# Kernel tuning notes

Hardware: AMD Instinct MI355X
Metric: run time of the kernel (lower is better)

Reference implementation:

```python
import jax, jax.numpy as jnp
import numpy as np

NUM_GROUPS = 32


def setup_inputs() -> dict:
    key = jax.random.key(0)
    x = jax.random.normal(key, (16384, 4096), dtype=jnp.float32)
    return {"x": x}


def reference(x):
    N, D = x.shape
    G = NUM_GROUPS
    d = D // G
    # [N, G, d] -> mean-center over batch
    xg = x.reshape(N, G, d)
    xg = xg - xg.mean(axis=0, keepdims=True)
    # [G, N, d]
    xg = jnp.transpose(xg, (1, 0, 2))
    # per-group covariance: [G, d, d]
    covs = jnp.einsum('gnd,gne->gde', xg, xg) / (N - 1)
    S, U = jnp.linalg.eigh(covs)  # S: [G, d], U: [G, d, d]
    # whitening transform W = U diag(S^-1/2) U^T : [G, d, d]
    W = jnp.einsum('gde,ge,gfe->gdf', U, jax.lax.rsqrt(S), U)
    out = jnp.einsum('gnd,gdf->gnf', xg, W)  # [G, N, d]
    return jnp.transpose(out, (1, 0, 2)).reshape(N, D)
```

## Files before the change

kernel.cpp:

```cpp
#include <hip/hip_runtime.h>
#include <cstddef>

#define NROWS 16384
#define NCOLS 4096
#define NG 32
#define GD 128
#define NPC 16

typedef float f32x4 __attribute__((ext_vector_type(4)));
typedef short bf16x8 __attribute__((ext_vector_type(8)));

__device__ inline unsigned short f2bf(float f) {
    unsigned int u = __builtin_bit_cast(unsigned int, f);
    u += 0x7fffu + ((u >> 16) & 1u);
    return (unsigned short)(u >> 16);
}

__global__ __launch_bounds__(512) void k_cov(
    const float* __restrict__ x, float* __restrict__ xtx, float* __restrict__ ps,
    unsigned short* __restrict__ xhi)
{
    __shared__ unsigned short xt[2][128][42];
    __shared__ float red[8][128];
    const int bid = blockIdx.x;
    const int g = bid >> 4, p = bid & 15;
    const int t = threadIdx.x;
    const int w = t >> 6;
    const int lane = t & 63;
    const int f2 = lane;
    const int lm = lane & 15, lk = lane >> 4;
    const float* xb = x + (size_t)(p * 1024) * NCOLS + g * GD + 2 * f2;
    unsigned int* xo = (unsigned int*)(xhi
        + ((size_t)g * NROWS + p * 1024 + w * 4) * GD + 2 * f2);

    float csum0 = 0.f, csum1 = 0.f;
    f32x4 acc[8];
#pragma unroll
    for (int ni = 0; ni < 8; ++ni) acc[ni] = (f32x4){0.f, 0.f, 0.f, 0.f};

    float2 v[4];
#define CLOAD(CC) \
    _Pragma("unroll") for (int i = 0; i < 4; ++i) \
        v[i] = *(const float2*)(xb + (size_t)((CC) * 32 + w * 4 + i) * NCOLS);
#define CWRITE(BUF, CC) { \
    ushort4 h0, h1; \
    unsigned short* hp0 = (unsigned short*)&h0; \
    unsigned short* hp1 = (unsigned short*)&h1; \
    _Pragma("unroll") for (int i = 0; i < 4; ++i) { \
        csum0 += v[i].x; csum1 += v[i].y; \
        unsigned int b0 = f2bf(v[i].x), b1 = f2bf(v[i].y); \
        hp0[i] = (unsigned short)b0; hp1[i] = (unsigned short)b1; \
        xo[(size_t)((CC) * 32 + i) * 64] = b0 | (b1 << 16); } \
    *(ushort4*)&xt[BUF][2 * f2][w * 4] = h0; \
    *(ushort4*)&xt[BUF][2 * f2 + 1][w * 4] = h1; }

    CLOAD(0);
    CWRITE(0, 0);
    __syncthreads();

    for (int c = 0; c < 32; ++c) {
        const int cur = c & 1;
        if (c < 31) { CLOAD(c + 1); }
        bf16x8 A0 = *(const bf16x8*)&xt[cur][w * 16 + lm][lk * 8];
        bf16x8 B[8];
#pragma unroll
        for (int n = 0; n < 8; ++n)
            B[n] = *(const bf16x8*)&xt[cur][n * 16 + lm][lk * 8];
#pragma unroll
        for (int n = 0; n < 8; ++n)
            acc[n] = __builtin_amdgcn_mfma_f32_16x16x32_bf16(A0, B[n], acc[n], 0, 0, 0);
        if (c < 31) { CWRITE(cur ^ 1, c + 1); }
        __syncthreads();
    }
#undef CLOAD
#undef CWRITE

    float* ob = xtx + (size_t)bid * (GD * GD);
#pragma unroll
    for (int ni = 0; ni < 8; ++ni) {
        const int i0 = w * 16 + lk * 4;
        const int j = ni * 16 + lm;
#pragma unroll
        for (int r = 0; r < 4; ++r)
            ob[(size_t)(i0 + r) * GD + j] = acc[ni][r];
    }
    red[w][2 * f2] = csum0;
    red[w][2 * f2 + 1] = csum1;
    __syncthreads();
    if (t < 128) {
        float s = 0.f;
#pragma unroll
        for (int r = 0; r < 8; ++r) s += red[r][t];
        ps[(size_t)bid * GD + t] = s;
    }
}

__global__ __launch_bounds__(256) void k_covreduce(
    const float* __restrict__ xtx, const float* __restrict__ ps,
    float* __restrict__ C)
{
    __shared__ float mu[128];
    const int bid = blockIdx.x;
    const int g = bid >> 4, s = bid & 15;
    const int t = threadIdx.x;
    if (t < 128) {
        float m = 0.f;
#pragma unroll
        for (int p = 0; p < NPC; ++p) m += ps[(size_t)(g * NPC + p) * GD + t];
        mu[t] = m * (1.0f / (float)NROWS);
    }
    __syncthreads();
    const int e = s * 1024 + t * 4;
    const int i = e >> 7, j = e & 127;
    float4 sum = make_float4(0.f, 0.f, 0.f, 0.f);
#pragma unroll
    for (int p = 0; p < NPC; ++p) {
        const float4 vv = *(const float4*)(xtx + ((size_t)(g * NPC + p) << 14) + e);
        sum.x += vv.x; sum.y += vv.y; sum.z += vv.z; sum.w += vv.w;
    }
    const float inv = 1.0f / (float)(NROWS - 1);
    const float mi2 = (float)NROWS * mu[i];
    float4 r;
    r.x = (sum.x - mi2 * mu[j + 0]) * inv;
    r.y = (sum.y - mi2 * mu[j + 1]) * inv;
    r.z = (sum.z - mi2 * mu[j + 2]) * inv;
    r.w = (sum.w - mi2 * mu[j + 3]) * inv;
    *(float4*)(C + (size_t)g * (GD * GD) + e) = r;
}

__global__ __launch_bounds__(256) void k_prep(
    const float* __restrict__ Cg, float* __restrict__ scale,
    float* __restrict__ Y0, float* __restrict__ Z0)
{
    __shared__ float Cs[128][129];
    __shared__ float rs[128];
    __shared__ float sinv[1];
    const int g = blockIdx.x;
    const int t = threadIdx.x;
    for (int k = 0; k < 64; ++k) {
        int e = t + 256 * k;
        Cs[e >> 7][e & 127] = Cg[(size_t)g * (GD * GD) + e];
    }
    __syncthreads();
    if (t < 128) {
        float s = 0.f;
        for (int i = 0; i < 128; ++i) s += fabsf(Cs[i][t]);
        rs[t] = s;
    }
    __syncthreads();
    if (t == 0) {
        float up = 0.f, lo = 1e30f;
        for (int i = 0; i < 128; ++i) {
            up = fmaxf(up, rs[i]);
            lo = fminf(lo, 2.0f * Cs[i][i] - rs[i]);
        }
        float c = 0.5f * (up + fmaxf(lo, 0.0f));
        c = fmaxf(c, 1e-20f);
        sinv[0] = 1.0f / c;
        scale[g] = rsqrtf(c);
    }
    __syncthreads();
    const float invc = sinv[0];
    for (int k = 0; k < 64; ++k) {
        int e = t + 256 * k;
        int i = e >> 7, j = e & 127;
        Y0[(size_t)g * (GD * GD) + e] = Cs[i][j] * invc;
        Z0[(size_t)g * (GD * GD) + e] = (i == j) ? 1.0f : 0.0f;
    }
}

__global__ __launch_bounds__(256) void k_ns_iter(
    const float* __restrict__ Yin, const float* __restrict__ Zin,
    float* __restrict__ Yout, float* __restrict__ Zout)
{
    __shared__ float Ys[128][132];
    __shared__ float Zs[128][132];
    __shared__ float Ts[128][16];
    const int bid = blockIdx.x;
    const int g = bid >> 3;
    const int sl = bid & 7;
    const int J0 = sl * 16;
    const int t = threadIdx.x;
    const float* Yg = Yin + (size_t)g * GD * GD;
    const float* Zg = Zin + (size_t)g * GD * GD;
#pragma unroll
    for (int k = 0; k < 16; ++k) {
        int q = t + 256 * k;
        int row = q >> 5, c4 = q & 31;
        *(float4*)&Ys[row][c4 * 4] = *(const float4*)(Yg + (size_t)q * 4);
        *(float4*)&Zs[row][c4 * 4] = *(const float4*)(Zg + (size_t)q * 4);
    }
    __syncthreads();
    const int i = t >> 1;
    const int jb = (t & 1) * 8;

    float accT[8];
#pragma unroll
    for (int q = 0; q < 8; ++q) accT[q] = 0.f;
    for (int k4 = 0; k4 < 32; ++k4) {
        float4 zv = *(const float4*)&Zs[i][k4 * 4];
        float zz[4] = {zv.x, zv.y, zv.z, zv.w};
#pragma unroll
        for (int e = 0; e < 4; ++e) {
            const int k = k4 * 4 + e;
            float4 y0 = *(const float4*)&Ys[k][J0 + jb];
            float4 y1 = *(const float4*)&Ys[k][J0 + jb + 4];
            float yy[8] = {y0.x, y0.y, y0.z, y0.w, y1.x, y1.y, y1.z, y1.w};
#pragma unroll
            for (int q = 0; q < 8; ++q) accT[q] = fmaf(zz[e], yy[q], accT[q]);
        }
    }
#pragma unroll
    for (int q = 0; q < 8; ++q) Ts[i][jb + q] = accT[q];
    __syncthreads();

    float ay[8], az[8];
#pragma unroll
    for (int q = 0; q < 8; ++q) { ay[q] = 0.f; az[q] = 0.f; }
    for (int k4 = 0; k4 < 32; ++k4) {
        float4 yv = *(const float4*)&Ys[i][k4 * 4];
        float4 zv = *(const float4*)&Zs[i][k4 * 4];
        float yy[4] = {yv.x, yv.y, yv.z, yv.w};
        float zz[4] = {zv.x, zv.y, zv.z, zv.w};
#pragma unroll
        for (int e = 0; e < 4; ++e) {
            const int k = k4 * 4 + e;
            float4 t0 = *(const float4*)&Ts[k][jb];
            float4 t1 = *(const float4*)&Ts[k][jb + 4];
            float tt[8] = {t0.x, t0.y, t0.z, t0.w, t1.x, t1.y, t1.z, t1.w};
#pragma unroll
            for (int q = 0; q < 8; ++q) {
                ay[q] = fmaf(yy[e], tt[q], ay[q]);
                az[q] = fmaf(zz[e], tt[q], az[q]);
            }
        }
    }
    float4 yc0 = *(const float4*)&Ys[i][J0 + jb];
    float4 yc1 = *(const float4*)&Ys[i][J0 + jb + 4];
    float4 zc0 = *(const float4*)&Zs[i][J0 + jb];
    float4 zc1 = *(const float4*)&Zs[i][J0 + jb + 4];
    float* Yo = Yout + (size_t)g * GD * GD + (size_t)i * GD + J0 + jb;
    float* Zo = Zout + (size_t)g * GD * GD + (size_t)i * GD + J0 + jb;
    *(float4*)(Yo)     = make_float4(1.5f*yc0.x - 0.5f*ay[0], 1.5f*yc0.y - 0.5f*ay[1],
                                     1.5f*yc0.z - 0.5f*ay[2], 1.5f*yc0.w - 0.5f*ay[3]);
    *(float4*)(Yo + 4) = make_float4(1.5f*yc1.x - 0.5f*ay[4], 1.5f*yc1.y - 0.5f*ay[5],
                                     1.5f*yc1.z - 0.5f*ay[6], 1.5f*yc1.w - 0.5f*ay[7]);
    *(float4*)(Zo)     = make_float4(1.5f*zc0.x - 0.5f*az[0], 1.5f*zc0.y - 0.5f*az[1],
                                     1.5f*zc0.z - 0.5f*az[2], 1.5f*zc0.w - 0.5f*az[3]);
    *(float4*)(Zo + 4) = make_float4(1.5f*zc1.x - 0.5f*az[4], 1.5f*zc1.y - 0.5f*az[5],
                                     1.5f*zc1.z - 0.5f*az[6], 1.5f*zc1.w - 0.5f*az[7]);
}

__global__ __launch_bounds__(256) void k_wprep(
    const float* __restrict__ Z, const float* __restrict__ scale,
    const float* __restrict__ ps,
    unsigned short* __restrict__ WT, float* __restrict__ muW)
{
    __shared__ float Zs[128][129];
    __shared__ float mu[128];
    const int g = blockIdx.x;
    const int t = threadIdx.x;
    const float sc = scale[g];
    if (t < 128) {
        float m = 0.f;
#pragma unroll
        for (int p = 0; p < NPC; ++p) m += ps[(size_t)(g * NPC + p) * GD + t];
        mu[t] = m * (1.0f / (float)NROWS);
    }
    for (int k = 0; k < 64; ++k) {
        int e = t + 256 * k;
        Zs[e >> 7][e & 127] = Z[(size_t)g * (GD * GD) + e];
    }
    __syncthreads();
    const int n = t & 127, kh = t >> 7;
    unsigned short* o = WT + (size_t)g * (GD * GD) + (size_t)n * GD + kh * 64;
    for (int k = 0; k < 64; k += 2) {
        unsigned int pk = (unsigned int)f2bf(Zs[kh * 64 + k][n] * sc)
                        | ((unsigned int)f2bf(Zs[kh * 64 + k + 1][n] * sc) << 16);
        *(unsigned int*)(o + k) = pk;
    }
    if (t < 128) {
        float s = 0.f;
        for (int d = 0; d < 128; ++d) s = fmaf(mu[d], Zs[d][t], s);
        muW[g * GD + t] = s * sc;
    }
}

__global__ __launch_bounds__(512) void k_apply(
    const unsigned short* __restrict__ xhi, const unsigned short* __restrict__ WT,
    const float* __restrict__ muW, float* __restrict__ out)
{
    __shared__ float tile[64][132];
    const int bid = blockIdx.x;
    const int g = bid & 31;
    const int rb = bid >> 5;
    const int t = threadIdx.x;
    const int lane = t & 63, w = t >> 6;
    const int lm = lane & 15, lk = lane >> 4;
    const int fq = w >> 1;
    const int sh = (w & 1) * 32;

    bf16x8 Wf[2][4];
    {
        const unsigned short* wg = WT + (size_t)g * (GD * GD);
#pragma unroll
        for (int fi = 0; fi < 2; ++fi)
#pragma unroll
            for (int ks = 0; ks < 4; ++ks)
                Wf[fi][ks] = *(const bf16x8*)(wg
                    + (size_t)(fq * 32 + fi * 16 + lm) * GD + ks * 32 + lk * 8);
    }
    float mw[2];
#pragma unroll
    for (int fi = 0; fi < 2; ++fi)
        mw[fi] = muW[g * GD + fq * 32 + fi * 16 + lm];

    const int row0 = rb * 64;
    const unsigned short* ab = xhi
        + ((size_t)g * NROWS + row0 + sh + lm) * GD + lk * 8;

    bf16x8 u[8];
#pragma unroll
    for (int ks = 0; ks < 4; ++ks) {
        u[ks * 2 + 0] = *(const bf16x8*)(ab + ks * 32);
        u[ks * 2 + 1] = *(const bf16x8*)(ab + (size_t)16 * GD + ks * 32);
    }

    f32x4 acc[2][2];
#pragma unroll
    for (int mi = 0; mi < 2; ++mi)
#pragma unroll
        for (int fi = 0; fi < 2; ++fi) acc[mi][fi] = (f32x4){0.f, 0.f, 0.f, 0.f};

#pragma unroll
    for (int ks = 0; ks < 4; ++ks) {
#pragma unroll
        for (int fi = 0; fi < 2; ++fi) {
            acc[0][fi] = __builtin_amdgcn_mfma_f32_16x16x32_bf16(
                u[ks * 2 + 0], Wf[fi][ks], acc[0][fi], 0, 0, 0);
            acc[1][fi] = __builtin_amdgcn_mfma_f32_16x16x32_bf16(
                u[ks * 2 + 1], Wf[fi][ks], acc[1][fi], 0, 0, 0);
        }
    }

#pragma unroll
    for (int mi = 0; mi < 2; ++mi)
#pragma unroll
        for (int fi = 0; fi < 2; ++fi)
#pragma unroll
            for (int r = 0; r < 4; ++r)
                tile[sh + mi * 16 + lk * 4 + r][fq * 32 + fi * 16 + lm]
                    = acc[mi][fi][r] - mw[fi];
    __syncthreads();

    const int srow = t >> 5;
    const int scol = (t & 31) * 4;
    float* obase = out + (size_t)row0 * NCOLS + g * GD;
#pragma unroll
    for (int p = 0; p < 4; ++p) {
        const int row = p * 16 + srow;
        float4 v = *(const float4*)&tile[row][scol];
        *(float4*)(obase + (size_t)row * NCOLS + scol) = v;
    }
}

extern "C" void kernel_launch(void* const* d_in, const int* in_sizes, int n_in,
                              void* d_out, int out_size, void* d_ws, size_t ws_size,
                              hipStream_t stream) {
    const float* x = (const float*)d_in[0];
    float* out = (float*)d_out;
    float* ws = (float*)d_ws;

    float* xtx   = ws;
    float* ps    = xtx + (size_t)NG * NPC * GD * GD;
    float* scale = ps + (size_t)NG * NPC * GD;
    float* Cbuf  = scale + 32;
    float* Ya    = Cbuf + (size_t)NG * GD * GD;
    float* Za    = Ya + (size_t)NG * GD * GD;
    float* Yb    = Za + (size_t)NG * GD * GD;
    float* Zb    = Yb + (size_t)NG * GD * GD;
    float* muW   = Zb + (size_t)NG * GD * GD;
    unsigned short* WT  = (unsigned short*)(muW + NCOLS);
    unsigned short* xhi = WT + (size_t)NG * GD * GD;

    k_cov<<<NG * NPC, 512, 0, stream>>>(x, xtx, ps, xhi);
    k_covreduce<<<NG * NPC, 256, 0, stream>>>(xtx, ps, Cbuf);
    k_prep<<<NG, 256, 0, stream>>>(Cbuf, scale, Ya, Za);
    for (int it = 0; it < 5; ++it) {
        if ((it & 1) == 0)
            k_ns_iter<<<NG * 8, 256, 0, stream>>>(Ya, Za, Yb, Zb);
        else
            k_ns_iter<<<NG * 8, 256, 0, stream>>>(Yb, Zb, Ya, Za);
    }
    k_wprep<<<NG, 256, 0, stream>>>(Zb, scale, ps, WT, muW);
    k_apply<<<NG * 256, 512, 0, stream>>>(xhi, WT, muW, out);
}
```

Measured before the change: 340.1 us.

## Drop bf16 staging copy of x; apply reads fp32 x directly, fewer NS iterations

The covariance kernel no longer writes a bf16 transposed copy of x. The apply kernel instead reads the fp32 input directly and converts it to bf16 in registers before the MFMA, with smaller 256-thread blocks covering 32 rows each. This removes a 128MB write and the matching read, at the cost of reading 256MB of fp32 in apply. Separately, the Newton-Schulz iteration count drops from 5 to 4, which cuts work but may reduce the accuracy of the inverse square root.

```diff
diff --git a/kernel.cpp b/kernel.cpp
--- a/kernel.cpp
+++ b/kernel.cpp
@@ -17,8 +17,7 @@
 }
 
 __global__ __launch_bounds__(512) void k_cov(
-    const float* __restrict__ x, float* __restrict__ xtx, float* __restrict__ ps,
-    unsigned short* __restrict__ xhi)
+    const float* __restrict__ x, float* __restrict__ xtx, float* __restrict__ ps)
 {
     __shared__ unsigned short xt[2][128][42];
     __shared__ float red[8][128];
@@ -30,8 +29,6 @@
     const int f2 = lane;
     const int lm = lane & 15, lk = lane >> 4;
     const float* xb = x + (size_t)(p * 1024) * NCOLS + g * GD + 2 * f2;
-    unsigned int* xo = (unsigned int*)(xhi
-        + ((size_t)g * NROWS + p * 1024 + w * 4) * GD + 2 * f2);
 
     float csum0 = 0.f, csum1 = 0.f;
     f32x4 acc[8];
@@ -42,20 +39,18 @@
 #define CLOAD(CC) \
     _Pragma("unroll") for (int i = 0; i < 4; ++i) \
         v[i] = *(const float2*)(xb + (size_t)((CC) * 32 + w * 4 + i) * NCOLS);
-#define CWRITE(BUF, CC) { \
+#define CWRITE(BUF) { \
     ushort4 h0, h1; \
     unsigned short* hp0 = (unsigned short*)&h0; \
     unsigned short* hp1 = (unsigned short*)&h1; \
     _Pragma("unroll") for (int i = 0; i < 4; ++i) { \
         csum0 += v[i].x; csum1 += v[i].y; \
-        unsigned int b0 = f2bf(v[i].x), b1 = f2bf(v[i].y); \
-        hp0[i] = (unsigned short)b0; hp1[i] = (unsigned short)b1; \
-        xo[(size_t)((CC) * 32 + i) * 64] = b0 | (b1 << 16); } \
+        hp0[i] = f2bf(v[i].x); hp1[i] = f2bf(v[i].y); } \
     *(ushort4*)&xt[BUF][2 * f2][w * 4] = h0; \
     *(ushort4*)&xt[BUF][2 * f2 + 1][w * 4] = h1; }
 
     CLOAD(0);
-    CWRITE(0, 0);
+    CWRITE(0);
     __syncthreads();
 
     for (int c = 0; c < 32; ++c) {
@@ -69,7 +64,7 @@
 #pragma unroll
         for (int n = 0; n < 8; ++n)
             acc[n] = __builtin_amdgcn_mfma_f32_16x16x32_bf16(A0, B[n], acc[n], 0, 0, 0);
-        if (c < 31) { CWRITE(cur ^ 1, c + 1); }
+        if (c < 31) { CWRITE(cur ^ 1); }
         __syncthreads();
     }
 #undef CLOAD
@@ -286,19 +281,18 @@
     }
 }
 
-__global__ __launch_bounds__(512) void k_apply(
-    const unsigned short* __restrict__ xhi, const unsigned short* __restrict__ WT,
+__global__ __launch_bounds__(256) void k_apply(
+    const float* __restrict__ x, const unsigned short* __restrict__ WT,
     const float* __restrict__ muW, float* __restrict__ out)
 {
-    __shared__ float tile[64][132];
+    __shared__ float tile[32][132];
     const int bid = blockIdx.x;
     const int g = bid & 31;
     const int rb = bid >> 5;
     const int t = threadIdx.x;
     const int lane = t & 63, w = t >> 6;
     const int lm = lane & 15, lk = lane >> 4;
-    const int fq = w >> 1;
-    const int sh = (w & 1) * 32;
+    const int fq = w;
 
     bf16x8 Wf[2][4];
     {
@@ -315,15 +309,16 @@
     for (int fi = 0; fi < 2; ++fi)
         mw[fi] = muW[g * GD + fq * 32 + fi * 16 + lm];
 
-    const int row0 = rb * 64;
-    const unsigned short* ab = xhi
-        + ((size_t)g * NROWS + row0 + sh + lm) * GD + lk * 8;
-
-    bf16x8 u[8];
+    const int row0 = rb * 32;
+    const float* ab = x + (size_t)(row0 + lm) * NCOLS + g * GD + lk * 8;
+
+    float4 u[16];
 #pragma unroll
     for (int ks = 0; ks < 4; ++ks) {
-        u[ks * 2 + 0] = *(const bf16x8*)(ab + ks * 32);
-        u[ks * 2 + 1] = *(const bf16x8*)(ab + (size_t)16 * GD + ks * 32);
+        u[ks * 4 + 0] = *(const float4*)(ab + ks * 32);
+        u[ks * 4 + 1] = *(const float4*)(ab + ks * 32 + 4);
+        u[ks * 4 + 2] = *(const float4*)(ab + (size_t)16 * NCOLS + ks * 32);
+        u[ks * 4 + 3] = *(const float4*)(ab + (size_t)16 * NCOLS + ks * 32 + 4);
     }
 
     f32x4 acc[2][2];
@@ -334,12 +329,23 @@
 
 #pragma unroll
     for (int ks = 0; ks < 4; ++ks) {
+        float4 q0 = u[ks * 4 + 0], q1 = u[ks * 4 + 1];
+        float4 q2 = u[ks * 4 + 2], q3 = u[ks * 4 + 3];
+        bf16x8 a0, a1;
+        a0[0] = (short)f2bf(q0.x); a0[1] = (short)f2bf(q0.y);
+        a0[2] = (short)f2bf(q0.z); a0[3] = (short)f2bf(q0.w);
+        a0[4] = (short)f2bf(q1.x); a0[5] = (short)f2bf(q1.y);
+        a0[6] = (short)f2bf(q1.z); a0[7] = (short)f2bf(q1.w);
+        a1[0] = (short)f2bf(q2.x); a1[1] = (short)f2bf(q2.y);
+        a1[2] = (short)f2bf(q2.z); a1[3] = (short)f2bf(q2.w);
+        a1[4] = (short)f2bf(q3.x); a1[5] = (short)f2bf(q3.y);
+        a1[6] = (short)f2bf(q3.z); a1[7] = (short)f2bf(q3.w);
 #pragma unroll
         for (int fi = 0; fi < 2; ++fi) {
             acc[0][fi] = __builtin_amdgcn_mfma_f32_16x16x32_bf16(
-                u[ks * 2 + 0], Wf[fi][ks], acc[0][fi], 0, 0, 0);
+                a0, Wf[fi][ks], acc[0][fi], 0, 0, 0);
             acc[1][fi] = __builtin_amdgcn_mfma_f32_16x16x32_bf16(
-                u[ks * 2 + 1], Wf[fi][ks], acc[1][fi], 0, 0, 0);
+                a1, Wf[fi][ks], acc[1][fi], 0, 0, 0);
         }
     }
 
@@ -349,7 +355,7 @@
         for (int fi = 0; fi < 2; ++fi)
 #pragma unroll
             for (int r = 0; r < 4; ++r)
-                tile[sh + mi * 16 + lk * 4 + r][fq * 32 + fi * 16 + lm]
+                tile[mi * 16 + lk * 4 + r][fq * 32 + fi * 16 + lm]
                     = acc[mi][fi][r] - mw[fi];
     __syncthreads();
 
@@ -358,9 +364,9 @@
     float* obase = out + (size_t)row0 * NCOLS + g * GD;
 #pragma unroll
     for (int p = 0; p < 4; ++p) {
-        const int row = p * 16 + srow;
-        float4 v = *(const float4*)&tile[row][scol];
-        *(float4*)(obase + (size_t)row * NCOLS + scol) = v;
+        const int row = p * 8 + srow;
+        float4 vv = *(const float4*)&tile[row][scol];
+        *(float4*)(obase + (size_t)row * NCOLS + scol) = vv;
     }
 }
 
@@ -380,18 +386,17 @@
     float* Yb    = Za + (size_t)NG * GD * GD;
     float* Zb    = Yb + (size_t)NG * GD * GD;
     float* muW   = Zb + (size_t)NG * GD * GD;
-    unsigned short* WT  = (unsigned short*)(muW + NCOLS);
-    unsigned short* xhi = WT + (size_t)NG * GD * GD;
-
-    k_cov<<<NG * NPC, 512, 0, stream>>>(x, xtx, ps, xhi);
+    unsigned short* WT = (unsigned short*)(muW + NCOLS);
+
+    k_cov<<<NG * NPC, 512, 0, stream>>>(x, xtx, ps);
     k_covreduce<<<NG * NPC, 256, 0, stream>>>(xtx, ps, Cbuf);
     k_prep<<<NG, 256, 0, stream>>>(Cbuf, scale, Ya, Za);
-    for (int it = 0; it < 5; ++it) {
+    for (int it = 0; it < 4; ++it) {
         if ((it & 1) == 0)
             k_ns_iter<<<NG * 8, 256, 0, stream>>>(Ya, Za, Yb, Zb);
         else
             k_ns_iter<<<NG * 8, 256, 0, stream>>>(Yb, Zb, Ya, Za);
     }
-    k_wprep<<<NG, 256, 0, stream>>>(Zb, scale, ps, WT, muW);
-    k_apply<<<NG * 256, 512, 0, stream>>>(xhi, WT, muW, out);
-}
+    k_wprep<<<NG, 256, 0, stream>>>(Za, scale, ps, WT, muW);
+    k_apply<<<NG * 512, 256, 0, stream>>>(x, WT, muW, out);
+}
```

Result: no change. 346.5 us (+1.9%).
